# Kernel tuning notes

Hardware: AMD Instinct MI355X
Metric: run time of the kernel (lower is better)

The kernel has to match this reference:

```python
import jax, jax.numpy as jnp
import numpy as np

N, D_IN = 65536, 512
X_DIMS = [512, 2048, 2048, 512]
Y_DIMS = [512, 1024, 512]
T = 2            # n_treatments
OUT_DIM = 1


def setup_inputs() -> dict:
    key = jax.random.key(0)
    ks = iter(jax.random.split(key, 32))
    s = 0.02
    inp = {
        "x": jax.random.normal(next(ks), (N, D_IN), dtype=jnp.float32),
        "treatment": jax.random.randint(next(ks), (N,), 0, T, dtype=jnp.int64),
        # shared trunk MLP (Linear+ReLU after EVERY linear, per original code)
        "Wx0": jax.random.normal(next(ks), (X_DIMS[0], X_DIMS[1]), jnp.float32) * s,
        "bx0": jnp.zeros((X_DIMS[1],), jnp.float32),
        "Wx1": jax.random.normal(next(ks), (X_DIMS[1], X_DIMS[2]), jnp.float32) * s,
        "bx1": jnp.zeros((X_DIMS[2],), jnp.float32),
        "Wx2": jax.random.normal(next(ks), (X_DIMS[2], X_DIMS[3]), jnp.float32) * s,
        "bx2": jnp.zeros((X_DIMS[3],), jnp.float32),
        # per-treatment expert MLPs, stacked on leading T axis
        "Wy0": jax.random.normal(next(ks), (T, Y_DIMS[0], Y_DIMS[1]), jnp.float32) * s,
        "by0": jnp.zeros((T, Y_DIMS[1]), jnp.float32),
        "Wy1": jax.random.normal(next(ks), (T, Y_DIMS[1], Y_DIMS[2]), jnp.float32) * s,
        "by1": jnp.zeros((T, Y_DIMS[2]), jnp.float32),
        # per-treatment output heads
        "Wo": jax.random.normal(next(ks), (T, Y_DIMS[2], OUT_DIM), jnp.float32) * s,
        "bo": jnp.zeros((T, OUT_DIM), jnp.float32),
        # propensity head
        "Wt": jax.random.normal(next(ks), (X_DIMS[3], 1), jnp.float32) * s,
        "bt": jnp.zeros((1,), jnp.float32),
    }
    return inp


def reference(x, treatment, Wx0, bx0, Wx1, bx1, Wx2, bx2,
              Wy0, by0, Wy1, by1, Wo, bo, Wt, bt):
    # shared trunk: ReLU follows every Linear (original MLP applies ReLU after
    # the last layer too, because `i < len(dims)-1` is always true in the loop)
    h = jax.nn.relu(x @ Wx0 + bx0)
    h = jax.nn.relu(h @ Wx1 + bx1)
    x_emb = jax.nn.relu(h @ Wx2 + bx2)            # [N, 512]

    # per-treatment experts computed densely, then gathered by treatment id.
    # This is the dense-equivalent of SplitStreams -> MLP -> GatherStreams:
    # GatherStreams sorts by original row index, so row n of the output is the
    # treatment-`t[n]` head applied to x_emb[n].
    g = jax.nn.relu(jnp.einsum('nd,tdh->nth', x_emb, Wy0) + by0)   # [N,T,1024]
    g = jax.nn.relu(jnp.einsum('nth,thk->ntk', g, Wy1) + by1)      # [N,T,512]
    y_all = jnp.einsum('ntk,tko->nto', g, Wo) + bo                 # [N,T,1]

    t_idx = treatment.astype(jnp.int32).reshape(-1)
    y = jnp.take_along_axis(y_all, t_idx[:, None, None], axis=1)[:, 0, :]  # [N,1]

    # softmax over a size-1 axis -> all ones, but kept faithful to the source
    t_out = jax.nn.softmax(x_emb @ Wt + bt, axis=1)                # [N,1]
    return y, x_emb, t_out
```

## Files before the change

### kernel.cpp

```cpp
#include <hip/hip_runtime.h>
#include <hip/hip_bf16.h>
#include <cstdint>

#define NROWS 65536
#define TTREAT 2

typedef __bf16 bf16x8 __attribute__((ext_vector_type(8)));
typedef float f32x4 __attribute__((ext_vector_type(4)));
typedef unsigned short u16;
typedef u16 u16x8 __attribute__((ext_vector_type(8)));

#define GLOBAL_AS __attribute__((address_space(1)))
#define LDS_AS __attribute__((address_space(3)))

__device__ __forceinline__ int swz_col(int col, int row) {
    return (col & ~63) | (((((col >> 3) & 7) ^ (row & 7)) << 3)) | (col & 7);
}

__device__ __forceinline__ u16 f32_to_bf16_bits(float f) {
    union { float f; uint32_t u; } v; v.f = f;
    uint32_t u = v.u;
    return (u16)((u + 0x7FFFu + ((u >> 16) & 1u)) >> 16);
}

__global__ void cvt_f32_bf16(const float4* __restrict__ src, u16x8* __restrict__ dst, int n8) {
    int i = blockIdx.x * blockDim.x + threadIdx.x;
    if (i >= n8) return;
    float4 a = src[2 * i], b = src[2 * i + 1];
    u16x8 r;
    r[0] = f32_to_bf16_bits(a.x); r[1] = f32_to_bf16_bits(a.y);
    r[2] = f32_to_bf16_bits(a.z); r[3] = f32_to_bf16_bits(a.w);
    r[4] = f32_to_bf16_bits(b.x); r[5] = f32_to_bf16_bits(b.y);
    r[6] = f32_to_bf16_bits(b.z); r[7] = f32_to_bf16_bits(b.w);
    int row = i >> 6;
    int j = (i & ~7) | ((i ^ row) & 7);
    dst[j] = r;
}

__global__ void transpose_w(const float* __restrict__ src, u16* __restrict__ dst, int K, int M) {
    __shared__ float tile[32][33];
    size_t boff = (size_t)blockIdx.z * K * M;
    src += boff; dst += boff;
    int m0 = blockIdx.x * 32, k0 = blockIdx.y * 32;
    int tx = threadIdx.x, ty = threadIdx.y;
#pragma unroll
    for (int i = 0; i < 32; i += 8)
        tile[ty + i][tx] = src[(size_t)(k0 + ty + i) * M + m0 + tx];
    __syncthreads();
#pragma unroll
    for (int i = 0; i < 32; i += 8) {
        int row = m0 + ty + i, col = k0 + tx;
        dst[(size_t)row * K + swz_col(col, row)] = f32_to_bf16_bits(tile[tx][ty + i]);
    }
}

__global__ void zero_cnt(int* cnt) {
    if (threadIdx.x < TTREAT) cnt[threadIdx.x] = 0;
}

__global__ void partition_rows(const int* __restrict__ treat, int* __restrict__ idx, int* __restrict__ cnt) {
    __shared__ int waveCnt1[4];
    __shared__ int blockBase[2];
    const int tid = threadIdx.x;
    const int i = blockIdx.x * 256 + tid;
    const int wave = tid >> 6, lane = tid & 63;
    const int t = treat[i];
    const unsigned long long m1 = __ballot(t == 1);
    const int n1 = __popcll(m1);
    if (lane == 0) waveCnt1[wave] = n1;
    __syncthreads();
    const int w0 = waveCnt1[0], w1 = waveCnt1[1], w2 = waveCnt1[2], w3 = waveCnt1[3];
    const int tot1 = w0 + w1 + w2 + w3;
    if (tid == 0) blockBase[0] = atomicAdd(&cnt[0], 256 - tot1);
    else if (tid == 64) blockBase[1] = atomicAdd(&cnt[1], tot1);
    __syncthreads();
    int waveOff1 = 0;
    if (wave > 0) waveOff1 += w0;
    if (wave > 1) waveOff1 += w1;
    if (wave > 2) waveOff1 += w2;
    const int below1 = (int)__popcll(m1 & ((1ull << lane) - 1ull));
    int pos;
    if (t == 1) pos = blockBase[1] + waveOff1 + below1;
    else        pos = blockBase[0] + (wave * 64 - waveOff1) + (lane - below1);
    idx[t * NROWS + pos] = i;
}

__global__ void init_outputs(const int* __restrict__ treat, const float* __restrict__ bo,
                             float* __restrict__ y, float* __restrict__ t_out) {
    int i = blockIdx.x * 256 + threadIdx.x;
    if (i < NROWS) { y[i] = bo[treat[i]]; t_out[i] = 1.0f; }
}

template <bool GATHER, bool WRITE_F32, bool FUSE_HEAD>
__global__ void gemm_bias_relu(const u16* __restrict__ A, const u16* __restrict__ Bt,
                               const float* __restrict__ bias,
                               u16* __restrict__ C, float* __restrict__ C32,
                               const int* __restrict__ idx, const int* __restrict__ cntp,
                               int nrows, int chunkStart, int maxRows, int K, int M,
                               const float* __restrict__ Wo, float* __restrict__ y) {
    int rows = (cntp ? *cntp : nrows) - chunkStart;
    if (rows > maxRows) rows = maxRows;
    int rowBase = blockIdx.y * 128;
    if (rows <= 0 || rowBase >= rows) return;
    int colBase = blockIdx.x * 128;

    __shared__ __align__(16) u16 As[128 * 64];
    __shared__ __align__(16) u16 Bs[128 * 64];

    const int tid = threadIdx.x;
    const int wave = tid >> 6, lane = tid & 63;
    const int quad = lane >> 4, l16 = lane & 15;
    const int wm = wave >> 1, wn = wave & 1;

    const int r0 = tid >> 3;
    const int kc = (tid & 7) * 8;

    size_t a_off[4], b_off[4];
#pragma unroll
    for (int it = 0; it < 4; ++it) {
        int r = rowBase + r0 + it * 32;
        if (GATHER) {
            int rc = r < rows ? r : (rows - 1);
            int g = idx[rc];
            int kcg = ((((tid & 7) ^ (r & 7) ^ (g & 7)) & 7) * 8);
            a_off[it] = (size_t)g * K + kcg;
        } else {
            a_off[it] = (size_t)r * K + kc;
        }
        int c = colBase + r0 + it * 32;
        b_off[it] = (size_t)c * K + kc;
    }

    f32x4 acc[4][4] = {};

    for (int k0 = 0; k0 < K; k0 += 64) {
        __syncthreads();
#pragma unroll
        for (int it = 0; it < 4; ++it) {
            __builtin_amdgcn_global_load_lds(
                (const GLOBAL_AS void*)(A + a_off[it] + k0),
                (LDS_AS void*)(&As[(it * 256 + wave * 64) * 8]), 16, 0, 0);
            __builtin_amdgcn_global_load_lds(
                (const GLOBAL_AS void*)(Bt + b_off[it] + k0),
                (LDS_AS void*)(&Bs[(it * 256 + wave * 64) * 8]), 16, 0, 0);
        }
        __syncthreads();
#pragma unroll
        for (int kk = 0; kk < 2; ++kk) {
            bf16x8 aF[4], bF[4];
            const int csw = ((kk * 4 + quad) ^ (l16 & 7)) * 8;
#pragma unroll
            for (int mi = 0; mi < 4; ++mi)
                aF[mi] = *(const bf16x8*)&As[(wm * 64 + mi * 16 + l16) * 64 + csw];
#pragma unroll
            for (int ni = 0; ni < 4; ++ni)
                bF[ni] = *(const bf16x8*)&Bs[(wn * 64 + ni * 16 + l16) * 64 + csw];
#pragma unroll
            for (int mi = 0; mi < 4; ++mi)
#pragma unroll
                for (int ni = 0; ni < 4; ++ni)
                    acc[mi][ni] = __builtin_amdgcn_mfma_f32_16x16x32_bf16(
                        aF[mi], bF[ni], acc[mi][ni], 0, 0, 0);
        }
    }

    float bv[4];
#pragma unroll
    for (int ni = 0; ni < 4; ++ni) bv[ni] = bias[colBase + wn * 64 + ni * 16 + l16];

    if (FUSE_HEAD) {
        float wv[4];
#pragma unroll
        for (int ni = 0; ni < 4; ++ni) wv[ni] = Wo[colBase + wn * 64 + ni * 16 + l16];
        float hs[4][4];
#pragma unroll
        for (int mi = 0; mi < 4; ++mi)
#pragma unroll
            for (int r = 0; r < 4; ++r) {
                float s = 0.f;
#pragma unroll
                for (int ni = 0; ni < 4; ++ni) {
                    float v = acc[mi][ni][r] + bv[ni];
                    v = v > 0.f ? v : 0.f;
                    s += v * wv[ni];
                }
                hs[mi][r] = s;
            }
#pragma unroll
        for (int mi = 0; mi < 4; ++mi)
#pragma unroll
            for (int r = 0; r < 4; ++r) {
                float s = hs[mi][r];
                s += __shfl_down(s, 8, 16);
                s += __shfl_down(s, 4, 16);
                s += __shfl_down(s, 2, 16);
                s += __shfl_down(s, 1, 16);
                if (l16 == 0) {
                    int row = rowBase + wm * 64 + mi * 16 + quad * 4 + r;
                    if (row < rows) atomicAdd(&y[idx[row]], s);
                }
            }
    } else {
#pragma unroll
        for (int mi = 0; mi < 4; ++mi) {
            int rloc = rowBase + wm * 64 + mi * 16 + quad * 4;
#pragma unroll
            for (int ni = 0; ni < 4; ++ni) {
                int col = colBase + wn * 64 + ni * 16 + l16;
#pragma unroll
                for (int r = 0; r < 4; ++r) {
                    int row = rloc + r;
                    if (row < rows) {
                        float v = acc[mi][ni][r] + bv[ni];
                        v = v > 0.f ? v : 0.f;
                        C[(size_t)row * M + swz_col(col, row)] = f32_to_bf16_bits(v);
                        if (WRITE_F32) C32[(size_t)row * M + col] = v;
                    }
                }
            }
        }
    }
}

extern "C" void kernel_launch(void* const* d_in, const int* in_sizes, int n_in,
                              void* d_out, int out_size, void* d_ws, size_t ws_size,
                              hipStream_t stream) {
    const float* x   = (const float*)d_in[0];
    const int* treat = (const int*)d_in[1];
    const float* Wx0 = (const float*)d_in[2];
    const float* bx0 = (const float*)d_in[3];
    const float* Wx1 = (const float*)d_in[4];
    const float* bx1 = (const float*)d_in[5];
    const float* Wx2 = (const float*)d_in[6];
    const float* bx2 = (const float*)d_in[7];
    const float* Wy0 = (const float*)d_in[8];
    const float* by0 = (const float*)d_in[9];
    const float* Wy1 = (const float*)d_in[10];
    const float* by1 = (const float*)d_in[11];
    const float* Wo  = (const float*)d_in[12];
    const float* bo  = (const float*)d_in[13];

    float* out_y  = (float*)d_out;
    float* out_xe = out_y + NROWS;
    float* out_t  = out_xe + (size_t)NROWS * 512;

    const size_t FIXED = ((size_t)(2048 * 512 + 2048 * 2048 + 512 * 2048
                          + TTREAT * 1024 * 512 + TTREAT * 512 * 1024
                          + (size_t)NROWS * 512) * 2)
                          + (size_t)TTREAT * NROWS * 4 + (1 << 20);
    int R = 512;
    const int cands[8] = {65536, 32768, 16384, 8192, 4096, 2048, 1024, 512};
    for (int ci = 0; ci < 8; ++ci) {
        if (FIXED + (size_t)cands[ci] * 11264 <= ws_size) { R = cands[ci]; break; }
    }
    const int NCHUNK = NROWS / R;

    size_t off = 0;
    auto carve = [&](size_t bytes) {
        void* p = (char*)d_ws + off;
        off += (bytes + 255) & ~(size_t)255;
        return p;
    };
    u16* Wx0t = (u16*)carve((size_t)2048 * 512 * 2);
    u16* Wx1t = (u16*)carve((size_t)2048 * 2048 * 2);
    u16* Wx2t = (u16*)carve((size_t)512 * 2048 * 2);
    u16* Wy0t = (u16*)carve((size_t)TTREAT * 1024 * 512 * 2);
    u16* Wy1t = (u16*)carve((size_t)TTREAT * 512 * 1024 * 2);
    u16* xe   = (u16*)carve((size_t)NROWS * 512 * 2);
    int* idx  = (int*)carve((size_t)TTREAT * NROWS * 4);
    int* cnt  = (int*)carve(256);
    u16* xbc  = (u16*)carve((size_t)R * 512 * 2);
    u16* h1c  = (u16*)carve((size_t)R * 2048 * 2);
    u16* h2c  = (u16*)carve((size_t)R * 2048 * 2);
    u16* g1c  = (u16*)carve((size_t)R * 1024 * 2);

    dim3 tb32(32, 8);

    transpose_w<<<dim3(2048 / 32, 512 / 32, 1), tb32, 0, stream>>>(Wx0, Wx0t, 512, 2048);
    transpose_w<<<dim3(2048 / 32, 2048 / 32, 1), tb32, 0, stream>>>(Wx1, Wx1t, 2048, 2048);
    transpose_w<<<dim3(512 / 32, 2048 / 32, 1), tb32, 0, stream>>>(Wx2, Wx2t, 2048, 512);
    transpose_w<<<dim3(1024 / 32, 512 / 32, TTREAT), tb32, 0, stream>>>(Wy0, Wy0t, 512, 1024);
    transpose_w<<<dim3(512 / 32, 1024 / 32, TTREAT), tb32, 0, stream>>>(Wy1, Wy1t, 1024, 512);

    zero_cnt<<<1, 64, 0, stream>>>(cnt);
    partition_rows<<<NROWS / 256, 256, 0, stream>>>(treat, idx, cnt);

    init_outputs<<<NROWS / 256, 256, 0, stream>>>(treat, bo, out_y, out_t);

    const int gy = R / 128;

    for (int c = 0; c < NCHUNK; ++c) {
        int cS = c * R;
        cvt_f32_bf16<<<(R * 512 / 8 + 255) / 256, 256, 0, stream>>>(
            (const float4*)(x + (size_t)cS * 512), (u16x8*)xbc, R * 512 / 8);
        gemm_bias_relu<false, false, false><<<dim3(2048 / 128, gy), 256, 0, stream>>>(
            xbc, Wx0t, bx0, h1c, nullptr, nullptr, nullptr, NROWS, cS, R, 512, 2048,
            nullptr, nullptr);
        gemm_bias_relu<false, false, false><<<dim3(2048 / 128, gy), 256, 0, stream>>>(
            h1c, Wx1t, bx1, h2c, nullptr, nullptr, nullptr, NROWS, cS, R, 2048, 2048,
            nullptr, nullptr);
        gemm_bias_relu<false, true, false><<<dim3(512 / 128, gy), 256, 0, stream>>>(
            h2c, Wx2t, bx2, xe + (size_t)cS * 512, out_xe + (size_t)cS * 512,
            nullptr, nullptr, NROWS, cS, R, 2048, 512, nullptr, nullptr);
    }

    for (int t = 0; t < TTREAT; ++t) {
        const int* idx_t = idx + (size_t)t * NROWS;
        for (int c = 0; c < NCHUNK; ++c) {
            int cS = c * R;
            gemm_bias_relu<true, false, false><<<dim3(1024 / 128, gy), 256, 0, stream>>>(
                xe, Wy0t + (size_t)t * 1024 * 512, by0 + (size_t)t * 1024,
                g1c, nullptr, idx_t + cS, cnt + t, NROWS, cS, R, 512, 1024,
                nullptr, nullptr);
            gemm_bias_relu<false, false, true><<<dim3(512 / 128, gy), 256, 0, stream>>>(
                g1c, Wy1t + (size_t)t * 512 * 1024, by1 + (size_t)t * 512,
                nullptr, nullptr, idx_t + cS, cnt + t, NROWS, cS, R, 1024, 512,
                Wo + (size_t)t * 512, out_y);
        }
    }
}
```

Measured before the change: 1.512 ms.

## Replace GEMM with 256x256 tile, 8-wave, double-buffered ping-pong pipelined kernel

Swaps the 128x128, 4-wave single-buffered GEMM for a 256x256 tile run by 8 waves. LDS is double-buffered, and global-to-LDS loads for the next K tiles are interleaved with four MFMA quadrants using explicit vmcnt waits, barriers and s_setprio. The aim is to hide load latency and raise arithmetic intensity per block. In exchange it needs 128KB of LDS and many more accumulator registers, and it launches far fewer blocks, which hurts the small-N GEMMs (512 wide) and the partially filled expert chunks.

Measured after the change: 1.719 ms. +13.7%, slower.

```diff
diff --git a/kernel.cpp b/kernel.cpp
--- a/kernel.cpp
+++ b/kernel.cpp
@@ -91,77 +91,165 @@
     if (i < NROWS) { y[i] = bo[treat[i]]; t_out[i] = 1.0f; }
 }
 
+#define BARX()    __asm__ __volatile__("s_barrier" ::: "memory")
+#define WAITVM(n) __asm__ __volatile__("s_waitcnt vmcnt(" #n ")" ::: "memory")
+
 template <bool GATHER, bool WRITE_F32, bool FUSE_HEAD>
-__global__ void gemm_bias_relu(const u16* __restrict__ A, const u16* __restrict__ Bt,
-                               const float* __restrict__ bias,
-                               u16* __restrict__ C, float* __restrict__ C32,
-                               const int* __restrict__ idx, const int* __restrict__ cntp,
-                               int nrows, int chunkStart, int maxRows, int K, int M,
-                               const float* __restrict__ Wo, float* __restrict__ y) {
+__global__ __launch_bounds__(512, 2)
+void gemm8p(const u16* __restrict__ A, const u16* __restrict__ Bt,
+            const float* __restrict__ bias,
+            u16* __restrict__ C, float* __restrict__ C32,
+            const int* __restrict__ idx, const int* __restrict__ cntp,
+            int nrows, int chunkStart, int maxRows, int K, int M,
+            const float* __restrict__ Wo, float* __restrict__ y) {
     int rows = (cntp ? *cntp : nrows) - chunkStart;
     if (rows > maxRows) rows = maxRows;
-    int rowBase = blockIdx.y * 128;
+    const int rowBase = blockIdx.y * 256;
     if (rows <= 0 || rowBase >= rows) return;
-    int colBase = blockIdx.x * 128;
-
-    __shared__ __align__(16) u16 As[128 * 64];
-    __shared__ __align__(16) u16 Bs[128 * 64];
-
-    const int tid = threadIdx.x;
+    const int colBase = blockIdx.x * 256;
+
+    __shared__ __align__(16) u16 As[2 * 16384];
+    __shared__ __align__(16) u16 Bs[2 * 16384];
+
+    const int tid  = threadIdx.x;
     const int wave = tid >> 6, lane = tid & 63;
     const int quad = lane >> 4, l16 = lane & 15;
-    const int wm = wave >> 1, wn = wave & 1;
-
-    const int r0 = tid >> 3;
-    const int kc = (tid & 7) * 8;
-
-    size_t a_off[4], b_off[4];
-#pragma unroll
-    for (int it = 0; it < 4; ++it) {
-        int r = rowBase + r0 + it * 32;
-        if (GATHER) {
-            int rc = r < rows ? r : (rows - 1);
-            int g = idx[rc];
-            int kcg = ((((tid & 7) ^ (r & 7) ^ (g & 7)) & 7) * 8);
-            a_off[it] = (size_t)g * K + kcg;
-        } else {
-            a_off[it] = (size_t)r * K + kc;
-        }
-        int c = colBase + r0 + it * 32;
-        b_off[it] = (size_t)c * K + kc;
-    }
-
-    f32x4 acc[4][4] = {};
-
-    for (int k0 = 0; k0 < K; k0 += 64) {
-        __syncthreads();
-#pragma unroll
-        for (int it = 0; it < 4; ++it) {
-            __builtin_amdgcn_global_load_lds(
-                (const GLOBAL_AS void*)(A + a_off[it] + k0),
-                (LDS_AS void*)(&As[(it * 256 + wave * 64) * 8]), 16, 0, 0);
-            __builtin_amdgcn_global_load_lds(
-                (const GLOBAL_AS void*)(Bt + b_off[it] + k0),
-                (LDS_AS void*)(&Bs[(it * 256 + wave * 64) * 8]), 16, 0, 0);
-        }
-        __syncthreads();
-#pragma unroll
-        for (int kk = 0; kk < 2; ++kk) {
-            bf16x8 aF[4], bF[4];
-            const int csw = ((kk * 4 + quad) ^ (l16 & 7)) * 8;
-#pragma unroll
-            for (int mi = 0; mi < 4; ++mi)
-                aF[mi] = *(const bf16x8*)&As[(wm * 64 + mi * 16 + l16) * 64 + csw];
-#pragma unroll
-            for (int ni = 0; ni < 4; ++ni)
-                bF[ni] = *(const bf16x8*)&Bs[(wn * 64 + ni * 16 + l16) * 64 + csw];
-#pragma unroll
-            for (int mi = 0; mi < 4; ++mi)
-#pragma unroll
-                for (int ni = 0; ni < 4; ++ni)
-                    acc[mi][ni] = __builtin_amdgcn_mfma_f32_16x16x32_bf16(
-                        aF[mi], bF[ni], acc[mi][ni], 0, 0, 0);
-        }
+    const int wm = wave >> 2, wn = wave & 3;
+    const int NT = K >> 6;
+
+    unsigned aoff[2][2], boff[2][2];
+#pragma unroll
+    for (int j = 0; j < 2; ++j)
+#pragma unroll
+        for (int h = 0; h < 2; ++h) {
+            int ci = j * 512 + tid;
+            int lr = h * 128 + (ci >> 3);
+            int p  = ci & 7;
+            if (GATHER) {
+                int r = rowBase + lr;
+                if (r >= rows) r = rows - 1;
+                int g = idx[r];
+                aoff[j][h] = (unsigned)g * (unsigned)K
+                           + (unsigned)(((p ^ (lr & 7) ^ (g & 7)) & 7) * 8);
+            } else {
+                aoff[j][h] = (unsigned)(rowBase + lr) * (unsigned)K + (unsigned)(p * 8);
+            }
+            boff[j][h] = (unsigned)(colBase + lr) * (unsigned)K + (unsigned)(p * 8);
+        }
+
+#define STAGE_A(buf, h, j, T_)                                                        \
+    __builtin_amdgcn_global_load_lds(                                                 \
+        (const GLOBAL_AS void*)(A + aoff[j][h] + (unsigned)(T_) * 64u),               \
+        (LDS_AS void*)(&As[(buf) * 16384 + (h) * 8192 + ((j) * 512 + wave * 64) * 8]),\
+        16, 0, 0)
+#define STAGE_B(buf, h, j, T_)                                                        \
+    __builtin_amdgcn_global_load_lds(                                                 \
+        (const GLOBAL_AS void*)(Bt + boff[j][h] + (unsigned)(T_) * 64u),              \
+        (LDS_AS void*)(&Bs[(buf) * 16384 + (h) * 8192 + ((j) * 512 + wave * 64) * 8]),\
+        16, 0, 0)
+
+    const int arow = wm * 128 + l16;
+    const int brow = wn * 64 + l16;
+    const int sl0 = ((0 + quad) ^ (l16 & 7)) * 8;
+    const int sl1 = ((4 + quad) ^ (l16 & 7)) * 8;
+
+#define RD_A(dst, mi, kk, buf) \
+    dst = *(const bf16x8*)&As[(buf) * 16384 + (arow + (mi) * 16) * 64 + ((kk) ? sl1 : sl0)]
+#define RD_B(dst, ni, kk, buf) \
+    dst = *(const bf16x8*)&Bs[(buf) * 16384 + (brow + (ni) * 16) * 64 + ((kk) ? sl1 : sl0)]
+#define MFMA_(c, a, b) c = __builtin_amdgcn_mfma_f32_16x16x32_bf16(a, b, c, 0, 0, 0)
+
+    f32x4 acc[8][4] = {};
+    bf16x8 aLo[4][2], aHi[4][2], bLo[2][2], bHi[2][2];
+
+#pragma unroll
+    for (int j = 0; j < 2; ++j) { STAGE_A(0, 0, j, 0); }
+#pragma unroll
+    for (int j = 0; j < 2; ++j) { STAGE_A(0, 1, j, 0); }
+#pragma unroll
+    for (int j = 0; j < 2; ++j) { STAGE_B(0, 0, j, 0); }
+#pragma unroll
+    for (int j = 0; j < 2; ++j) { STAGE_B(0, 1, j, 0); }
+#pragma unroll
+    for (int j = 0; j < 2; ++j) { STAGE_A(1, 0, j, 1); }
+#pragma unroll
+    for (int j = 0; j < 2; ++j) { STAGE_A(1, 1, j, 1); }
+#pragma unroll
+    for (int j = 0; j < 2; ++j) { STAGE_B(1, 0, j, 1); }
+    WAITVM(6);
+    BARX();
+#pragma unroll
+    for (int mi = 0; mi < 4; ++mi) { RD_A(aLo[mi][0], mi, 0, 0); RD_A(aLo[mi][1], mi, 1, 0); }
+#pragma unroll
+    for (int ni = 0; ni < 2; ++ni) { RD_B(bLo[ni][0], ni, 0, 0); RD_B(bLo[ni][1], ni, 1, 0); }
+
+#pragma unroll 2
+    for (int T = 0; T < NT; ++T) {
+        const int bc = T & 1, bn = bc ^ 1;
+#pragma unroll
+        for (int mi = 0; mi < 4; ++mi) { RD_A(aHi[mi][0], mi + 4, 0, bc); RD_A(aHi[mi][1], mi + 4, 1, bc); }
+#pragma unroll
+        for (int ni = 0; ni < 2; ++ni) { RD_B(bHi[ni][0], ni + 2, 0, bc); RD_B(bHi[ni][1], ni + 2, 1, bc); }
+        if (T + 1 < NT) { STAGE_B(bn, 1, 0, T + 1); STAGE_B(bn, 1, 1, T + 1); }
+        BARX();
+        __builtin_amdgcn_s_setprio(1);
+#pragma unroll
+        for (int mi = 0; mi < 4; ++mi)
+#pragma unroll
+            for (int ni = 0; ni < 2; ++ni) {
+                MFMA_(acc[mi][ni], aLo[mi][0], bLo[ni][0]);
+                MFMA_(acc[mi][ni], aLo[mi][1], bLo[ni][1]);
+            }
+        __builtin_amdgcn_s_setprio(0);
+        BARX();
+        __builtin_amdgcn_s_setprio(1);
+#pragma unroll
+        for (int mi = 0; mi < 4; ++mi)
+#pragma unroll
+            for (int ni = 0; ni < 2; ++ni) {
+                MFMA_(acc[mi][ni + 2], aLo[mi][0], bHi[ni][0]);
+                MFMA_(acc[mi][ni + 2], aLo[mi][1], bHi[ni][1]);
+            }
+        __builtin_amdgcn_s_setprio(0);
+        WAITVM(4);
+        BARX();
+        if (T + 1 < NT) {
+#pragma unroll
+            for (int mi = 0; mi < 4; ++mi) { RD_A(aLo[mi][0], mi, 0, bn); RD_A(aLo[mi][1], mi, 1, bn); }
+        }
+        if (T + 2 < NT) { STAGE_A(bc, 0, 0, T + 2); STAGE_A(bc, 0, 1, T + 2); }
+        BARX();
+        __builtin_amdgcn_s_setprio(1);
+#pragma unroll
+        for (int mi = 0; mi < 4; ++mi)
+#pragma unroll
+            for (int ni = 0; ni < 2; ++ni) {
+                MFMA_(acc[mi + 4][ni], aHi[mi][0], bLo[ni][0]);
+                MFMA_(acc[mi + 4][ni], aHi[mi][1], bLo[ni][1]);
+            }
+        __builtin_amdgcn_s_setprio(0);
+        WAITVM(2);
+        BARX();
+        if (T + 1 < NT) {
+#pragma unroll
+            for (int ni = 0; ni < 2; ++ni) { RD_B(bLo[ni][0], ni, 0, bn); RD_B(bLo[ni][1], ni, 1, bn); }
+        }
+        if (T + 2 < NT) {
+            STAGE_A(bc, 1, 0, T + 2); STAGE_A(bc, 1, 1, T + 2);
+            STAGE_B(bc, 0, 0, T + 2); STAGE_B(bc, 0, 1, T + 2);
+        }
+        BARX();
+        __builtin_amdgcn_s_setprio(1);
+#pragma unroll
+        for (int mi = 0; mi < 4; ++mi)
+#pragma unroll
+            for (int ni = 0; ni < 2; ++ni) {
+                MFMA_(acc[mi + 4][ni + 2], aHi[mi][0], bHi[ni][0]);
+                MFMA_(acc[mi + 4][ni + 2], aHi[mi][1], bHi[ni][1]);
+            }
+        __builtin_amdgcn_s_setprio(0);
+        WAITVM(6);
+        BARX();
     }
 
     float bv[4];
@@ -172,9 +260,8 @@
         float wv[4];
 #pragma unroll
         for (int ni = 0; ni < 4; ++ni) wv[ni] = Wo[colBase + wn * 64 + ni * 16 + l16];
-        float hs[4][4];
-#pragma unroll
-        for (int mi = 0; mi < 4; ++mi)
+#pragma unroll
+        for (int mi = 0; mi < 8; ++mi)
 #pragma unroll
             for (int r = 0; r < 4; ++r) {
                 float s = 0.f;
@@ -184,26 +271,19 @@
                     v = v > 0.f ? v : 0.f;
                     s += v * wv[ni];
                 }
-                hs[mi][r] = s;
-            }
-#pragma unroll
-        for (int mi = 0; mi < 4; ++mi)
-#pragma unroll
-            for (int r = 0; r < 4; ++r) {
-                float s = hs[mi][r];
                 s += __shfl_down(s, 8, 16);
                 s += __shfl_down(s, 4, 16);
                 s += __shfl_down(s, 2, 16);
                 s += __shfl_down(s, 1, 16);
                 if (l16 == 0) {
-                    int row = rowBase + wm * 64 + mi * 16 + quad * 4 + r;
+                    int row = rowBase + wm * 128 + mi * 16 + quad * 4 + r;
                     if (row < rows) atomicAdd(&y[idx[row]], s);
                 }
             }
     } else {
 #pragma unroll
-        for (int mi = 0; mi < 4; ++mi) {
-            int rloc = rowBase + wm * 64 + mi * 16 + quad * 4;
+        for (int mi = 0; mi < 8; ++mi) {
+            int rloc = rowBase + wm * 128 + mi * 16 + quad * 4;
 #pragma unroll
             for (int ni = 0; ni < 4; ++ni) {
                 int col = colBase + wn * 64 + ni * 16 + l16;
@@ -220,6 +300,11 @@
             }
         }
     }
+#undef STAGE_A
+#undef STAGE_B
+#undef RD_A
+#undef RD_B
+#undef MFMA_
 }
 
 extern "C" void kernel_launch(void* const* d_in, const int* in_sizes, int n_in,
@@ -287,19 +372,19 @@
 
     init_outputs<<<NROWS / 256, 256, 0, stream>>>(treat, bo, out_y, out_t);
 
-    const int gy = R / 128;
+    const int gy = R / 256;
 
     for (int c = 0; c < NCHUNK; ++c) {
         int cS = c * R;
         cvt_f32_bf16<<<(R * 512 / 8 + 255) / 256, 256, 0, stream>>>(
             (const float4*)(x + (size_t)cS * 512), (u16x8*)xbc, R * 512 / 8);
-        gemm_bias_relu<false, false, false><<<dim3(2048 / 128, gy), 256, 0, stream>>>(
+        gemm8p<false, false, false><<<dim3(2048 / 256, gy), 512, 0, stream>>>(
             xbc, Wx0t, bx0, h1c, nullptr, nullptr, nullptr, NROWS, cS, R, 512, 2048,
             nullptr, nullptr);
-        gemm_bias_relu<false, false, false><<<dim3(2048 / 128, gy), 256, 0, stream>>>(
+        gemm8p<false, false, false><<<dim3(2048 / 256, gy), 512, 0, stream>>>(
             h1c, Wx1t, bx1, h2c, nullptr, nullptr, nullptr, NROWS, cS, R, 2048, 2048,
             nullptr, nullptr);
-        gemm_bias_relu<false, true, false><<<dim3(512 / 128, gy), 256, 0, stream>>>(
+        gemm8p<false, true, false><<<dim3(512 / 256, gy), 512, 0, stream>>>(
             h2c, Wx2t, bx2, xe + (size_t)cS * 512, out_xe + (size_t)cS * 512,
             nullptr, nullptr, NROWS, cS, R, 2048, 512, nullptr, nullptr);
     }
@@ -308,11 +393,11 @@
         const int* idx_t = idx + (size_t)t * NROWS;
         for (int c = 0; c < NCHUNK; ++c) {
             int cS = c * R;
-            gemm_bias_relu<true, false, false><<<dim3(1024 / 128, gy), 256, 0, stream>>>(
+            gemm8p<true, false, false><<<dim3(1024 / 256, gy), 512, 0, stream>>>(
                 xe, Wy0t + (size_t)t * 1024 * 512, by0 + (size_t)t * 1024,
                 g1c, nullptr, idx_t + cS, cnt + t, NROWS, cS, R, 512, 1024,
                 nullptr, nullptr);
-            gemm_bias_relu<false, false, true><<<dim3(512 / 128, gy), 256, 0, stream>>>(
+            gemm8p<false, false, true><<<dim3(512 / 256, gy), 512, 0, stream>>>(
                 g1c, Wy1t + (size_t)t * 512 * 1024, by1 + (size_t)t * 512,
                 nullptr, nullptr, idx_t + cS, cnt + t, NROWS, cS, R, 1024, 512,
                 Wo + (size_t)t * 512, out_y);
```
